# Kernel optimization log

Hardware: AMD Instinct MI355X
Metric: run time of the kernel (lower is better)

## Reference

```python
import jax, jax.numpy as jnp
import numpy as np

D_MODEL, H, D_FF = 512, 8, 2048
DK = D_MODEL // H
EPS = 1e-5  # torch LayerNorm default


def layer_norm(x, g, b):
    m = jnp.mean(x, axis=-1, keepdims=True)
    v = jnp.mean((x - m) ** 2, axis=-1, keepdims=True)
    return (x - m) * jax.lax.rsqrt(v + EPS) * g + b


def setup_inputs() -> dict:
    key = jax.random.key(0)
    ks = jax.random.split(key, 10)
    B, S = 8, 2048
    s = lambda fan_in: 1.0 / np.sqrt(fan_in)
    return {
        "x": jax.random.normal(ks[0], (B, S, D_MODEL), jnp.float32),
        # per-head projections stacked: [h, d_model, dk] (bias-free Project)
        "wq": jax.random.uniform(ks[1], (H, D_MODEL, DK), jnp.float32, -s(D_MODEL), s(D_MODEL)),
        "wk": jax.random.uniform(ks[2], (H, D_MODEL, DK), jnp.float32, -s(D_MODEL), s(D_MODEL)),
        "wv": jax.random.uniform(ks[3], (H, D_MODEL, DK), jnp.float32, -s(D_MODEL), s(D_MODEL)),
        "wo": jax.random.uniform(ks[4], (D_MODEL, D_MODEL), jnp.float32, -s(D_MODEL), s(D_MODEL)),
        "w1": jax.random.uniform(ks[5], (D_MODEL, D_FF), jnp.float32, -s(D_MODEL), s(D_MODEL)),
        "b1": jax.random.uniform(ks[6], (D_FF,), jnp.float32, -s(D_MODEL), s(D_MODEL)),
        "w2": jax.random.uniform(ks[7], (D_FF, D_MODEL), jnp.float32, -s(D_FF), s(D_FF)),
        "b2": jax.random.uniform(ks[8], (D_MODEL,), jnp.float32, -s(D_FF), s(D_FF)),
        "ln1_g": jnp.ones((D_MODEL,), jnp.float32),
        "ln1_b": jnp.zeros((D_MODEL,), jnp.float32),
        "ln2_g": jnp.ones((D_MODEL,), jnp.float32),
        "ln2_b": jnp.zeros((D_MODEL,), jnp.float32),
    }


def reference(x, wq, wk, wv, wo, w1, b1, w2, b2, ln1_g, ln1_b, ln2_g, ln2_b):
    B, S, D = x.shape
    # --- multi-head self-attention (8 per-head Linears fused into one einsum) ---
    q = jnp.einsum("bsd,hdk->bhsk", x, wq)
    k = jnp.einsum("bsd,hdk->bhsk", x, wk)
    v = jnp.einsum("bsd,hdk->bhsk", x, wv)
    score = jnp.einsum("bhsk,bhtk->bhst", q, k) * (1.0 / np.sqrt(DK))
    attn = jax.nn.softmax(score, axis=-1)
    heads = jnp.einsum("bhst,bhtk->bhsk", attn, v)
    concat = heads.transpose(0, 2, 1, 3).reshape(B, S, D)  # cat over heads
    mha = concat @ wo
    # dropout in eval mode -> identity
    x = layer_norm(mha + x, ln1_g, ln1_b)
    # --- feed-forward ---
    ffn = jax.nn.relu(x @ w1 + b1) @ w2 + b2
    return layer_norm(ffn + x, ln2_g, ln2_b)
```

## Files before the change

kernel.cpp:

```cpp
#include <hip/hip_runtime.h>
#include <hip/hip_bf16.h>
#include <math.h>


#define D_MODEL 512
#define NHEAD   8
#define DKH     64
#define SEQ     2048
#define BATCH   8
#define DFF     2048
#define MROWS   (BATCH * SEQ)
#define QKVLD   1536

typedef __bf16 bf16x8 __attribute__((ext_vector_type(8)));
typedef float  f32x4  __attribute__((ext_vector_type(4)));
typedef float  f32x16 __attribute__((ext_vector_type(16)));

__device__ __forceinline__ unsigned short f2bf(float f) {
    union { float f; unsigned u; } v; v.f = f;
    return (unsigned short)((v.u + 0x7FFFu + ((v.u >> 16) & 1u)) >> 16);
}

__device__ __forceinline__ float bf2f(unsigned short u) {
    union { unsigned u; float f; } v; v.u = (unsigned)u << 16;
    return v.f;
}

__device__ __forceinline__ unsigned cvtpk(float a, float b) {
    unsigned r;
    asm("v_cvt_pk_bf16_f32 %0, %1, %2" : "=v"(r) : "v"(a), "v"(b));
    return r;
}

__device__ __forceinline__ float fexp2(float x) {
    float r; asm("v_exp_f32 %0, %1" : "=v"(r) : "v"(x)); return r;
}

__device__ __forceinline__ void plswap(unsigned& x, unsigned& y) {
    asm volatile("v_permlane32_swap_b32 %0, %1" : "+v"(x), "+v"(y));
}

__device__ __forceinline__ unsigned fbits(float f) {
    union { float f; unsigned u; } v; v.f = f; return v.u;
}
__device__ __forceinline__ float bitsf(unsigned u) {
    union { unsigned u; float f; } v; v.u = u; return v.f;
}

__device__ __forceinline__ f32x4 mfma16(bf16x8 a, bf16x8 b, f32x4 c) {
    return __builtin_amdgcn_mfma_f32_16x16x32_bf16(a, b, c, 0, 0, 0);
}
__device__ __forceinline__ f32x16 mfma32(bf16x8 a, bf16x8 b, f32x16 c) {
    return __builtin_amdgcn_mfma_f32_32x32x16_bf16(a, b, c, 0, 0, 0);
}

__device__ __forceinline__ void gld_lds16(const unsigned short* g, unsigned short* l) {
    __builtin_amdgcn_global_load_lds(
        (const __attribute__((address_space(1))) unsigned int*)g,
        (__attribute__((address_space(3))) unsigned int*)l, 16, 0, 0);
}

template<bool BIAS, bool RELU, int RESMODE, bool OUTF32>
__global__ __launch_bounds__(256)
void mfma_gemm(const unsigned short* __restrict__ Av,
               const unsigned short* __restrict__ Bt,
               const float* __restrict__ bias, const void* __restrict__ resv,
               void* __restrict__ Cv, int Kdim, int lda, int ldc)
{
    __shared__ unsigned short As[2][128][32];
    __shared__ unsigned short Bs[2][128][32];

    const int tid  = threadIdx.x;
    const int lane = tid & 63;
    const int w    = tid >> 6;
    const int mq   = (w >> 1) << 6;
    const int nq   = (w & 1) << 6;
    const int lrow = lane & 15;
    const int g    = lane >> 4;
    const int lk   = g << 3;

    const int row0 = blockIdx.y << 7;
    const int col0 = blockIdx.x << 7;

    const int c0   = w << 5;
    const int srow = lane >> 2;
    const int scol = (lane & 3) << 3;
    const size_t aoff = (size_t)(row0 + c0 + srow) * lda  + scol;
    const size_t boff = (size_t)(col0 + c0 + srow) * Kdim + scol;

    auto stage = [&](int buf, int kt) {
        gld_lds16(Av + aoff + kt,                        &As[buf][c0     ][0]);
        gld_lds16(Av + aoff + (size_t)16 * lda  + kt,    &As[buf][c0 + 16][0]);
        gld_lds16(Bt + boff + kt,                        &Bs[buf][c0     ][0]);
        gld_lds16(Bt + boff + (size_t)16 * Kdim + kt,    &Bs[buf][c0 + 16][0]);
    };

    const f32x4 zero = {0.f, 0.f, 0.f, 0.f};
    f32x4 acc[4][4];
    #pragma unroll
    for (int i = 0; i < 4; ++i)
        #pragma unroll
        for (int j = 0; j < 4; ++j) acc[i][j] = zero;

    stage(0, 0);
    __syncthreads();

    int cur = 0;
    for (int kt = 0; kt < Kdim; kt += 32) {
        if (kt + 32 < Kdim) stage(cur ^ 1, kt + 32);

        bf16x8 af[4], bfv[4];
        #pragma unroll
        for (int mf = 0; mf < 4; ++mf)
            af[mf] = *(const bf16x8*)&As[cur][mq + mf * 16 + lrow][lk];
        #pragma unroll
        for (int nf = 0; nf < 4; ++nf)
            bfv[nf] = *(const bf16x8*)&Bs[cur][nq + nf * 16 + lrow][lk];
        #pragma unroll
        for (int mf = 0; mf < 4; ++mf)
            #pragma unroll
            for (int nf = 0; nf < 4; ++nf)
                acc[mf][nf] = mfma16(af[mf], bfv[nf], acc[mf][nf]);

        __syncthreads();
        cur ^= 1;
    }

    const int orow = row0 + mq + g * 4;
    const int ocol = col0 + nq + lrow;
    #pragma unroll
    for (int mf = 0; mf < 4; ++mf) {
        #pragma unroll
        for (int nf = 0; nf < 4; ++nf) {
            const int cc = ocol + nf * 16;
            float bv = 0.f;
            if constexpr (BIAS) bv = bias[cc];
            float v[4];
            #pragma unroll
            for (int r = 0; r < 4; ++r) {
                const int rr = orow + mf * 16 + r;
                v[r] = acc[mf][nf][r];
                if constexpr (BIAS) v[r] += bv;
                if constexpr (RELU) v[r] = fmaxf(v[r], 0.f);
                if constexpr (RESMODE == 1)
                    v[r] += ((const float*)resv)[(size_t)rr * ldc + cc];
                if constexpr (RESMODE == 2)
                    v[r] += bf2f(((const unsigned short*)resv)[(size_t)rr * ldc + cc]);
                if constexpr (OUTF32) ((float*)Cv)[(size_t)rr * ldc + cc] = v[r];
            }
            if constexpr (!OUTF32) {
                const unsigned u01 = cvtpk(v[0], v[1]);
                const unsigned u23 = cvtpk(v[2], v[3]);
                unsigned short* cp = (unsigned short*)Cv + (size_t)(orow + mf * 16) * ldc + cc;
                cp[0]                 = (unsigned short)u01;
                cp[(size_t)ldc]       = (unsigned short)(u01 >> 16);
                cp[(size_t)ldc * 2]   = (unsigned short)u23;
                cp[(size_t)ldc * 3]   = (unsigned short)(u23 >> 16);
            }
        }
    }
}

__global__ __launch_bounds__(512, 4)
void mfma_attn(unsigned short* __restrict__ qkv)
{
    __shared__ unsigned short Ks[2][64][72];
    __shared__ unsigned short Vt[2][64][72];

    const int tid  = threadIdx.x;
    const int lane = tid & 63;
    const int w    = tid >> 6;
    const int q32  = lane & 31;
    const int h    = lane >> 5;

    const int bid  = blockIdx.x;
    const int idx  = bid >> 3;
    const int bh   = (bid & 7) * 8 + (idx & 7);
    const int b  = bh >> 3, hd = bh & 7;
    const int s0 = (idx >> 3) << 8;

    unsigned short* qptr = qkv + ((size_t)(b * SEQ + s0)) * QKVLD + hd * DKH;
    const unsigned short* kbase = qkv + ((size_t)(b * SEQ)) * QKVLD + 512 + hd * DKH;
    const unsigned short* vbase = qkv + ((size_t)(b * SEQ)) * QKVLD + 1024 + hd * DKH;

    bf16x8 qf[4];
    {
        const unsigned short* qp = qptr + (size_t)(w * 32 + q32) * QKVLD + 8 * h;
        #pragma unroll
        for (int t = 0; t < 4; ++t)
            qf[t] = *(const bf16x8*)(qp + 16 * t);
    }

    f32x16 z16;
    #pragma unroll
    for (int i = 0; i < 16; ++i) z16[i] = 0.f;

    const int kr = tid >> 3, kc = (tid & 7) << 3;
    const int vr = tid & 63, vc = (tid >> 6) << 3;

    uint4 kreg, vreg;
    auto loadKV = [&](int t0) {
        kreg = *(const uint4*)(kbase + (size_t)(t0 + kr) * QKVLD + kc);
        vreg = *(const uint4*)(vbase + (size_t)(t0 + vr) * QKVLD + vc);
    };
    loadKV(0);

    f32x16 oacc0, oacc1;
    #pragma unroll
    for (int i = 0; i < 16; ++i) { oacc0[i] = 0.f; oacc1[i] = 0.f; }
    float m = -INFINITY, lsum = 0.f;

    for (int t0 = 0; t0 < SEQ; t0 += 64) {
        const int cur = (t0 >> 6) & 1;
        *(uint4*)&Ks[cur][kr][kc] = kreg;
        {
            const unsigned short* vu = (const unsigned short*)&vreg;
            #pragma unroll
            for (int j = 0; j < 8; ++j) Vt[cur][vc + j][vr] = vu[j];
        }
        __syncthreads();

        if (t0 + 64 < SEQ) loadKV(t0 + 64);

        f32x16 sa0, sa1;
        __builtin_amdgcn_s_setprio(1);
        {
            const bf16x8 k0 = *(const bf16x8*)&Ks[cur][q32     ][8 * h];
            const bf16x8 k1 = *(const bf16x8*)&Ks[cur][32 + q32][8 * h];
            sa0 = mfma32(k0, qf[0], z16);
            sa1 = mfma32(k1, qf[0], z16);
        }
        #pragma unroll
        for (int t = 1; t < 4; ++t) {
            const bf16x8 k0 = *(const bf16x8*)&Ks[cur][q32     ][16 * t + 8 * h];
            const bf16x8 k1 = *(const bf16x8*)&Ks[cur][32 + q32][16 * t + 8 * h];
            sa0 = mfma32(k0, qf[t], sa0);
            sa1 = mfma32(k1, qf[t], sa1);
        }
        __builtin_amdgcn_s_setprio(0);

        float pmax = fmaxf(sa0[0], sa1[0]);
        #pragma unroll
        for (int r = 1; r < 16; ++r)
            pmax = fmaxf(pmax, fmaxf(sa0[r], sa1[r]));
        if (__any(pmax > m + 8.f)) {
            unsigned xx = fbits(pmax), yy = xx;
            plswap(xx, yy);
            const float partner = (lane < 32) ? bitsf(yy) : bitsf(xx);
            pmax = fmaxf(pmax, partner);
            const float mnew = fmaxf(m, pmax);
            const float alpha = fexp2(m - mnew);
            m = mnew;
            lsum *= alpha;
            #pragma unroll
            for (int r = 0; r < 16; ++r) {
                const int qr = (r & 3) + 8 * (r >> 2) + 4 * h;
                const float ar = __shfl(alpha, qr, 64);
                oacc0[r] *= ar;
                oacc1[r] *= ar;
            }
        }
        #pragma unroll
        for (int r = 0; r < 16; ++r) {
            sa0[r] = fexp2(sa0[r] - m);
            sa1[r] = fexp2(sa1[r] - m);
            lsum += sa0[r] + sa1[r];
        }

        bf16x8 pa[4];
        #pragma unroll
        for (int blk = 0; blk < 2; ++blk) {
            const f32x16& p = blk ? sa1 : sa0;
            #pragma unroll
            for (int tt = 0; tt < 2; ++tt) {
                unsigned a0 = cvtpk(p[8 * tt + 0], p[8 * tt + 1]);
                unsigned a1 = cvtpk(p[8 * tt + 2], p[8 * tt + 3]);
                unsigned b0 = cvtpk(p[8 * tt + 4], p[8 * tt + 5]);
                unsigned b1 = cvtpk(p[8 * tt + 6], p[8 * tt + 7]);
                plswap(a0, b0);
                plswap(a1, b1);
                union { uint4 u; bf16x8 v; } cvt;
                cvt.u.x = a0; cvt.u.y = a1; cvt.u.z = b0; cvt.u.w = b1;
                pa[blk * 2 + tt] = cvt.v;
            }
        }

        __builtin_amdgcn_s_setprio(1);
        #pragma unroll
        for (int ttg = 0; ttg < 4; ++ttg) {
            const bf16x8 vf0 = *(const bf16x8*)&Vt[cur][q32     ][16 * ttg + 8 * h];
            const bf16x8 vf1 = *(const bf16x8*)&Vt[cur][32 + q32][16 * ttg + 8 * h];
            oacc0 = mfma32(pa[ttg], vf0, oacc0);
            oacc1 = mfma32(pa[ttg], vf1, oacc1);
        }
        __builtin_amdgcn_s_setprio(0);
    }

    float ltot;
    {
        unsigned x = fbits(lsum), y = x;
        plswap(x, y);
        const float partner = (lane < 32) ? bitsf(y) : bitsf(x);
        ltot = lsum + partner;
    }
    const float inv = 1.f / ltot;
    #pragma unroll
    for (int r = 0; r < 16; ++r) {
        const int qr = (r & 3) + 8 * (r >> 2) + 4 * h;
        const float invr = __shfl(inv, qr, 64);
        unsigned short* op = qptr + (size_t)(w * 32 + qr) * QKVLD + q32;
        op[0]  = f2bf(oacc0[r] * invr);
        op[32] = f2bf(oacc1[r] * invr);
    }
}

template<bool WF32, bool WB16>
__global__ __launch_bounds__(256)
void ln_kernel(const float* __restrict__ in, const float* __restrict__ gg,
               const float* __restrict__ bb, float* __restrict__ outf,
               unsigned short* __restrict__ outb)
{
    const int row = blockIdx.x * 4 + (threadIdx.x >> 6);
    const int lane = threadIdx.x & 63;
    const float* p = in + (size_t)row * D_MODEL;

    const float4 a = *(const float4*)(p + lane * 4);
    const float4 c = *(const float4*)(p + 256 + lane * 4);
    float sum = a.x + a.y + a.z + a.w + c.x + c.y + c.z + c.w;
    float sq  = a.x*a.x + a.y*a.y + a.z*a.z + a.w*a.w
              + c.x*c.x + c.y*c.y + c.z*c.z + c.w*c.w;
    #pragma unroll
    for (int msk = 1; msk < 64; msk <<= 1) {
        sum += __shfl_xor(sum, msk, 64);
        sq  += __shfl_xor(sq,  msk, 64);
    }
    const float mean = sum * (1.f / 512.f);
    const float var  = sq * (1.f / 512.f) - mean * mean;
    const float rs   = rsqrtf(var + 1e-5f);

    const float4 g0 = *(const float4*)(gg + lane * 4);
    const float4 g1 = *(const float4*)(gg + 256 + lane * 4);
    const float4 b0 = *(const float4*)(bb + lane * 4);
    const float4 b1 = *(const float4*)(bb + 256 + lane * 4);

    float4 o0, o1;
    o0.x = (a.x - mean) * rs * g0.x + b0.x;
    o0.y = (a.y - mean) * rs * g0.y + b0.y;
    o0.z = (a.z - mean) * rs * g0.z + b0.z;
    o0.w = (a.w - mean) * rs * g0.w + b0.w;
    o1.x = (c.x - mean) * rs * g1.x + b1.x;
    o1.y = (c.y - mean) * rs * g1.y + b1.y;
    o1.z = (c.z - mean) * rs * g1.z + b1.z;
    o1.w = (c.w - mean) * rs * g1.w + b1.w;
    if constexpr (WF32) {
        *(float4*)(outf + (size_t)row * D_MODEL + lane * 4) = o0;
        *(float4*)(outf + (size_t)row * D_MODEL + 256 + lane * 4) = o1;
    }
    if constexpr (WB16) {
        uint2 pa, pb;
        pa.x = cvtpk(o0.x, o0.y);
        pa.y = cvtpk(o0.z, o0.w);
        pb.x = cvtpk(o1.x, o1.y);
        pb.y = cvtpk(o1.z, o1.w);
        *(uint2*)(outb + (size_t)row * D_MODEL + lane * 4) = pa;
        *(uint2*)(outb + (size_t)row * D_MODEL + 256 + lane * 4) = pb;
    }
}

__global__ __launch_bounds__(256)
void cast_bf16(const float* __restrict__ in, unsigned short* __restrict__ out)
{
    const size_t i = ((size_t)blockIdx.x * 256 + threadIdx.x) * 8;
    const float4 a = *(const float4*)(in + i);
    const float4 b = *(const float4*)(in + i + 4);
    uint4 o;
    o.x = cvtpk(a.x, a.y);
    o.y = cvtpk(a.z, a.w);
    o.z = cvtpk(b.x, b.y);
    o.w = cvtpk(b.z, b.w);
    *(uint4*)(out + i) = o;
}

__global__ __launch_bounds__(256)
void pack_qkv(const float* __restrict__ wq, const float* __restrict__ wk,
              const float* __restrict__ wv, unsigned short* __restrict__ Wqkv)
{
    const int idx = blockIdx.x * 256 + threadIdx.x;
    const int n = idx >> 9, d = idx & 511;
    const int h = n >> 6, c = n & 63;
    const size_t src = ((size_t)h * 512 + d) * 64 + c;
    Wqkv[idx]                 = f2bf(wq[src] * 0.18033688f);
    Wqkv[idx + 512 * 512]     = f2bf(wk[src]);
    Wqkv[idx + 2 * 512 * 512] = f2bf(wv[src]);
}

__global__ __launch_bounds__(256)
void pack_t(const float* __restrict__ in, unsigned short* __restrict__ out,
            int K, int N)
{
    __shared__ float t[32][33];
    const int kb = blockIdx.x << 5, nb = blockIdx.y << 5;
    const int c = threadIdx.x & 31, r0 = threadIdx.x >> 5;
    #pragma unroll
    for (int j = 0; j < 32; j += 8)
        t[r0 + j][c] = in[(size_t)(kb + r0 + j) * N + nb + c];
    __syncthreads();
    #pragma unroll
    for (int j = 0; j < 32; j += 8)
        out[(size_t)(nb + r0 + j) * K + kb + c] = f2bf(t[c][r0 + j]);
}

extern "C" void kernel_launch(void* const* d_in, const int* in_sizes, int n_in,
                              void* d_out, int out_size, void* d_ws, size_t ws_size,
                              hipStream_t stream)
{
    (void)in_sizes; (void)n_in; (void)out_size;

    const float* x    = (const float*)d_in[0];
    const float* wq   = (const float*)d_in[1];
    const float* wk   = (const float*)d_in[2];
    const float* wv   = (const float*)d_in[3];
    const float* wo   = (const float*)d_in[4];
    const float* w1   = (const float*)d_in[5];
    const float* b1   = (const float*)d_in[6];
    const float* w2   = (const float*)d_in[7];
    const float* b2   = (const float*)d_in[8];
    const float* ln1g = (const float*)d_in[9];
    const float* ln1b = (const float*)d_in[10];
    const float* ln2g = (const float*)d_in[11];
    const float* ln2b = (const float*)d_in[12];
    float* out = (float*)d_out;

    const size_t QKV_BYTES = (size_t)MROWS * QKVLD * 2;
    const size_t Y_BYTES   = (size_t)MROWS * D_MODEL * 4;
    unsigned char* base = (unsigned char*)d_ws;
    unsigned short* qkv  = (unsigned short*)(base);
    float*          y    = (float*)(base + QKV_BYTES);
    unsigned short* Wqkv = (unsigned short*)(base + QKV_BYTES + Y_BYTES);
    unsigned short* wo_t = Wqkv + 3 * 512 * 512;
    unsigned short* w1_t = wo_t + 512 * 512;
    unsigned short* w2_t = w1_t + 2048 * 512;
    unsigned short* hid  = w2_t + 2048 * 512;

    const size_t hid_off = (size_t)((unsigned char*)hid - base);
    const size_t avail = (ws_size > hid_off) ? (ws_size - hid_off) : 0;
    int chunk = (int)(avail / ((size_t)DFF * 2));
    chunk &= ~127;
    if (chunk > MROWS) chunk = MROWS;
    if (chunk < 128)   chunk = 128;

    float* y2 = (float*)qkv;
    unsigned short* xb  = (unsigned short*)d_out;
    unsigned short* x1b = (unsigned short*)d_out;

    pack_qkv<<<1024, 256, 0, stream>>>(wq, wk, wv, Wqkv);
    pack_t<<<dim3(16, 16), 256, 0, stream>>>(wo, wo_t, 512, 512);
    pack_t<<<dim3(16, 64), 256, 0, stream>>>(w1, w1_t, 512, 2048);
    pack_t<<<dim3(64, 16), 256, 0, stream>>>(w2, w2_t, 2048, 512);
    cast_bf16<<<(MROWS * D_MODEL) / (256 * 8), 256, 0, stream>>>(x, xb);

    const dim3 blk(256);

    mfma_gemm<false, false, 0, false>
        <<<dim3(12, MROWS / 128), blk, 0, stream>>>(xb, Wqkv, nullptr, nullptr,
                                                    qkv, 512, 512, QKVLD);

    mfma_attn<<<dim3(512), dim3(512), 0, stream>>>(qkv);

    mfma_gemm<false, false, 1, true>
        <<<dim3(4, MROWS / 128), blk, 0, stream>>>(qkv, wo_t, nullptr, x, y,
                                                   512, QKVLD, 512);

    ln_kernel<false, true><<<MROWS / 4, blk, 0, stream>>>(y, ln1g, ln1b,
                                                          nullptr, x1b);

    for (int r0 = 0; r0 < MROWS; r0 += chunk) {
        const int rows = (r0 + chunk <= MROWS) ? chunk : (MROWS - r0);
        mfma_gemm<true, true, 0, false>
            <<<dim3(DFF / 128, rows / 128), blk, 0, stream>>>(
                x1b + (size_t)r0 * D_MODEL, w1_t, b1, nullptr, hid,
                512, 512, DFF);
        mfma_gemm<true, false, 2, true>
            <<<dim3(4, rows / 128), blk, 0, stream>>>(
                hid, w2_t, b2, x1b + (size_t)r0 * D_MODEL,
                y2 + (size_t)r0 * D_MODEL, DFF, DFF, 512);
    }

    ln_kernel<true, false><<<MROWS / 4, blk, 0, stream>>>(y2, ln2g, ln2b,
                                                          out, nullptr);
}
```

Before: 292.5 us.

## Store pre-LayerNorm residual sums in bf16 and merge prep kernels into one launch

The output-projection and FFN2 GEMMs now write their residual-added results in bf16 instead of fp32, and both LayerNorm kernels read bf16 input. This halves the intermediate write and read traffic around each LayerNorm. The five weight-packing and input-cast kernels are merged into one launch that dispatches on block index, removing launch overhead. The cost is extra rounding of the pre-normalization activations, which reduces accuracy.

```diff
diff --git a/kernel.cpp b/kernel.cpp
--- a/kernel.cpp
+++ b/kernel.cpp
@@ -314,18 +314,30 @@
     }
 }
 
-template<bool WF32, bool WB16>
+template<bool INF32, bool WF32, bool WB16>
 __global__ __launch_bounds__(256)
-void ln_kernel(const float* __restrict__ in, const float* __restrict__ gg,
+void ln_kernel(const void* __restrict__ inv_, const float* __restrict__ gg,
                const float* __restrict__ bb, float* __restrict__ outf,
                unsigned short* __restrict__ outb)
 {
     const int row = blockIdx.x * 4 + (threadIdx.x >> 6);
     const int lane = threadIdx.x & 63;
-    const float* p = in + (size_t)row * D_MODEL;
-
-    const float4 a = *(const float4*)(p + lane * 4);
-    const float4 c = *(const float4*)(p + 256 + lane * 4);
+
+    float4 a, c;
+    if constexpr (INF32) {
+        const float* p = (const float*)inv_ + (size_t)row * D_MODEL;
+        a = *(const float4*)(p + lane * 4);
+        c = *(const float4*)(p + 256 + lane * 4);
+    } else {
+        const unsigned short* p = (const unsigned short*)inv_ + (size_t)row * D_MODEL;
+        const uint2 ua = *(const uint2*)(p + lane * 4);
+        const uint2 uc = *(const uint2*)(p + 256 + lane * 4);
+        a.x = bf2f((unsigned short)ua.x); a.y = bf2f((unsigned short)(ua.x >> 16));
+        a.z = bf2f((unsigned short)ua.y); a.w = bf2f((unsigned short)(ua.y >> 16));
+        c.x = bf2f((unsigned short)uc.x); c.y = bf2f((unsigned short)(uc.x >> 16));
+        c.z = bf2f((unsigned short)uc.y); c.w = bf2f((unsigned short)(uc.y >> 16));
+    }
+
     float sum = a.x + a.y + a.z + a.w + c.x + c.y + c.z + c.w;
     float sq  = a.x*a.x + a.y*a.y + a.z*a.z + a.w*a.w
               + c.x*c.x + c.y*c.y + c.z*c.z + c.w*c.w;
@@ -368,46 +380,51 @@
 }
 
 __global__ __launch_bounds__(256)
-void cast_bf16(const float* __restrict__ in, unsigned short* __restrict__ out)
-{
-    const size_t i = ((size_t)blockIdx.x * 256 + threadIdx.x) * 8;
-    const float4 a = *(const float4*)(in + i);
-    const float4 b = *(const float4*)(in + i + 4);
-    uint4 o;
-    o.x = cvtpk(a.x, a.y);
-    o.y = cvtpk(a.z, a.w);
-    o.z = cvtpk(b.x, b.y);
-    o.w = cvtpk(b.z, b.w);
-    *(uint4*)(out + i) = o;
-}
-
-__global__ __launch_bounds__(256)
-void pack_qkv(const float* __restrict__ wq, const float* __restrict__ wk,
-              const float* __restrict__ wv, unsigned short* __restrict__ Wqkv)
-{
-    const int idx = blockIdx.x * 256 + threadIdx.x;
-    const int n = idx >> 9, d = idx & 511;
-    const int h = n >> 6, c = n & 63;
-    const size_t src = ((size_t)h * 512 + d) * 64 + c;
-    Wqkv[idx]                 = f2bf(wq[src] * 0.18033688f);
-    Wqkv[idx + 512 * 512]     = f2bf(wk[src]);
-    Wqkv[idx + 2 * 512 * 512] = f2bf(wv[src]);
-}
-
-__global__ __launch_bounds__(256)
-void pack_t(const float* __restrict__ in, unsigned short* __restrict__ out,
-            int K, int N)
+void prep_all(const float* __restrict__ x,  const float* __restrict__ wq,
+              const float* __restrict__ wk, const float* __restrict__ wv,
+              const float* __restrict__ wo, const float* __restrict__ w1,
+              const float* __restrict__ w2,
+              unsigned short* __restrict__ xb, unsigned short* __restrict__ Wqkv,
+              unsigned short* __restrict__ wo_t, unsigned short* __restrict__ w1_t,
+              unsigned short* __restrict__ w2_t)
 {
     __shared__ float t[32][33];
-    const int kb = blockIdx.x << 5, nb = blockIdx.y << 5;
-    const int c = threadIdx.x & 31, r0 = threadIdx.x >> 5;
-    #pragma unroll
-    for (int j = 0; j < 32; j += 8)
-        t[r0 + j][c] = in[(size_t)(kb + r0 + j) * N + nb + c];
-    __syncthreads();
-    #pragma unroll
-    for (int j = 0; j < 32; j += 8)
-        out[(size_t)(nb + r0 + j) * K + kb + c] = f2bf(t[c][r0 + j]);
+    const int bid = blockIdx.x;
+
+    if (bid < 4096) {
+        const size_t i = ((size_t)bid * 256 + threadIdx.x) * 8;
+        const float4 a = *(const float4*)(x + i);
+        const float4 b = *(const float4*)(x + i + 4);
+        uint4 o;
+        o.x = cvtpk(a.x, a.y);
+        o.y = cvtpk(a.z, a.w);
+        o.z = cvtpk(b.x, b.y);
+        o.w = cvtpk(b.z, b.w);
+        *(uint4*)(xb + i) = o;
+    } else if (bid < 5120) {
+        const int idx = (bid - 4096) * 256 + threadIdx.x;
+        const int n = idx >> 9, d = idx & 511;
+        const int h = n >> 6, c = n & 63;
+        const size_t src = ((size_t)h * 512 + d) * 64 + c;
+        Wqkv[idx]                 = f2bf(wq[src] * 0.18033688f);
+        Wqkv[idx + 512 * 512]     = f2bf(wk[src]);
+        Wqkv[idx + 2 * 512 * 512] = f2bf(wv[src]);
+    } else {
+        const float* in; unsigned short* outp; int K, N, b;
+        if (bid < 5376)      { in = wo; outp = wo_t; K = 512;  N = 512;  b = bid - 5120; }
+        else if (bid < 6400) { in = w1; outp = w1_t; K = 512;  N = 2048; b = bid - 5376; }
+        else                 { in = w2; outp = w2_t; K = 2048; N = 512;  b = bid - 6400; }
+        const int gx = K >> 5;
+        const int kb = (b % gx) << 5, nb = (b / gx) << 5;
+        const int c = threadIdx.x & 31, r0 = threadIdx.x >> 5;
+        #pragma unroll
+        for (int j = 0; j < 32; j += 8)
+            t[r0 + j][c] = in[(size_t)(kb + r0 + j) * N + nb + c];
+        __syncthreads();
+        #pragma unroll
+        for (int j = 0; j < 32; j += 8)
+            outp[(size_t)(nb + r0 + j) * K + kb + c] = f2bf(t[c][r0 + j]);
+    }
 }
 
 extern "C" void kernel_launch(void* const* d_in, const int* in_sizes, int n_in,
@@ -435,7 +452,7 @@
     const size_t Y_BYTES   = (size_t)MROWS * D_MODEL * 4;
     unsigned char* base = (unsigned char*)d_ws;
     unsigned short* qkv  = (unsigned short*)(base);
-    float*          y    = (float*)(base + QKV_BYTES);
+    unsigned short* yb   = (unsigned short*)(base + QKV_BYTES);
     unsigned short* Wqkv = (unsigned short*)(base + QKV_BYTES + Y_BYTES);
     unsigned short* wo_t = Wqkv + 3 * 512 * 512;
     unsigned short* w1_t = wo_t + 512 * 512;
@@ -449,15 +466,12 @@
     if (chunk > MROWS) chunk = MROWS;
     if (chunk < 128)   chunk = 128;
 
-    float* y2 = (float*)qkv;
+    unsigned short* y2b = qkv;
     unsigned short* xb  = (unsigned short*)d_out;
     unsigned short* x1b = (unsigned short*)d_out;
 
-    pack_qkv<<<1024, 256, 0, stream>>>(wq, wk, wv, Wqkv);
-    pack_t<<<dim3(16, 16), 256, 0, stream>>>(wo, wo_t, 512, 512);
-    pack_t<<<dim3(16, 64), 256, 0, stream>>>(w1, w1_t, 512, 2048);
-    pack_t<<<dim3(64, 16), 256, 0, stream>>>(w2, w2_t, 2048, 512);
-    cast_bf16<<<(MROWS * D_MODEL) / (256 * 8), 256, 0, stream>>>(x, xb);
+    prep_all<<<7424, 256, 0, stream>>>(x, wq, wk, wv, wo, w1, w2,
+                                       xb, Wqkv, wo_t, w1_t, w2_t);
 
     const dim3 blk(256);
 
@@ -467,12 +481,12 @@
 
     mfma_attn<<<dim3(512), dim3(512), 0, stream>>>(qkv);
 
-    mfma_gemm<false, false, 1, true>
-        <<<dim3(4, MROWS / 128), blk, 0, stream>>>(qkv, wo_t, nullptr, x, y,
+    mfma_gemm<false, false, 1, false>
+        <<<dim3(4, MROWS / 128), blk, 0, stream>>>(qkv, wo_t, nullptr, x, yb,
                                                    512, QKVLD, 512);
 
-    ln_kernel<false, true><<<MROWS / 4, blk, 0, stream>>>(y, ln1g, ln1b,
-                                                          nullptr, x1b);
+    ln_kernel<false, false, true><<<MROWS / 4, blk, 0, stream>>>(
+        yb, ln1g, ln1b, nullptr, x1b);
 
     for (int r0 = 0; r0 < MROWS; r0 += chunk) {
         const int rows = (r0 + chunk <= MROWS) ? chunk : (MROWS - r0);
@@ -480,12 +494,12 @@
             <<<dim3(DFF / 128, rows / 128), blk, 0, stream>>>(
                 x1b + (size_t)r0 * D_MODEL, w1_t, b1, nullptr, hid,
                 512, 512, DFF);
-        mfma_gemm<true, false, 2, true>
+        mfma_gemm<true, false, 2, false>
             <<<dim3(4, rows / 128), blk, 0, stream>>>(
                 hid, w2_t, b2, x1b + (size_t)r0 * D_MODEL,
-                y2 + (size_t)r0 * D_MODEL, DFF, DFF, 512);
-    }
-
-    ln_kernel<true, false><<<MROWS / 4, blk, 0, stream>>>(y2, ln2g, ln2b,
-                                                          out, nullptr);
-}
+                y2b + (size_t)r0 * D_MODEL, DFF, DFF, 512);
+    }
+
+    ln_kernel<false, true, false><<<MROWS / 4, blk, 0, stream>>>(
+        y2b, ln2g, ln2b, out, nullptr);
+}
```

Result: faster. 280.9 us, median of 2 (-4.0%).
